# Performance work log

Measured on AMD Instinct MI355X. Metric: run time of the kernel, lower is better.

## Reference

```python
import jax, jax.numpy as jnp
import numpy as np

C = 1024
FACTOR = 4
C_INT = C * FACTOR


def setup_inputs() -> dict:
    key = jax.random.key(0)
    ks = jax.random.split(key, 6)
    act = jax.random.normal(ks[0], (4, 2048, C), dtype=jnp.float32)
    mask = jnp.ones((4, 2048), dtype=jnp.float32)
    # LayerNorm params
    ln_scale = jnp.ones((C,), dtype=jnp.float32)
    ln_bias = jnp.zeros((C,), dtype=jnp.float32)
    # Linear 1 (init='linear'): lecun-normal-ish
    w1 = jax.random.normal(ks[1], (C, C_INT), dtype=jnp.float32) / np.sqrt(C)
    b1 = jnp.zeros((C_INT,), dtype=jnp.float32)
    # Linear 2 (init='final' -> zeros in AF2; use small random so grads are nontrivial)
    w2 = jax.random.normal(ks[2], (C_INT, C), dtype=jnp.float32) * 0.02
    b2 = jnp.zeros((C,), dtype=jnp.float32)
    return {"act": act, "mask": mask, "ln_scale": ln_scale, "ln_bias": ln_bias,
            "w1": w1, "b1": b1, "w2": w2, "b2": b2}


def _layernorm(x, scale, bias, eps=1e-5):
    mu = jnp.mean(x, axis=-1, keepdims=True)
    var = jnp.mean(jnp.square(x - mu), axis=-1, keepdims=True)
    return (x - mu) * jax.lax.rsqrt(var + eps) * scale + bias


def reference(act, mask, ln_scale, ln_bias, w1, b1, w2, b2):
    # mask is accepted but unused, matching the original forward.
    x = _layernorm(act, ln_scale, ln_bias)
    h = jax.nn.relu(jnp.einsum('bsc,cf->bsf', x, w1) + b1)
    return jnp.einsum('bsf,fc->bsc', h, w2) + b2
```

## Files before the change

kernel.cpp:

```cpp
#include <hip/hip_runtime.h>
#include <hip/hip_bf16.h>
#include <cstdint>

typedef unsigned short u16;
typedef __bf16 bf16x8 __attribute__((ext_vector_type(8)));
typedef float floatx4 __attribute__((ext_vector_type(4)));

#define AS1 __attribute__((address_space(1)))
#define AS3 __attribute__((address_space(3)))

#define SCHED0  __builtin_amdgcn_sched_barrier(0)
#define BARRIER __builtin_amdgcn_s_barrier()

static __device__ __forceinline__ u16 f2bf(float f) {
    union { float f; unsigned int u; } v; v.f = f;
    unsigned int u = v.u;
    return (u16)((u + 0x7FFFu + ((u >> 16) & 1u)) >> 16);
}

__device__ __forceinline__ void transpose_body(
    const float* __restrict__ in, u16* __restrict__ out,
    int R, int Ccols, int bx, int by, int tid, float (*tile)[33])
{
    const int tx = tid & 31;
    const int ty = tid >> 5;
    const int c0 = bx * 32;
    const int r0 = by * 32;
#pragma unroll
    for (int i = 0; i < 32; i += 8)
        tile[ty + i][tx] = in[(size_t)(r0 + ty + i) * Ccols + (c0 + tx)];
    __syncthreads();
#pragma unroll
    for (int i = 0; i < 32; i += 8)
        out[(size_t)(c0 + ty + i) * R + (r0 + tx)] = f2bf(tile[tx][ty + i]);
}

__global__ __launch_bounds__(256)
void prep(const float* __restrict__ w1, const float* __restrict__ w2,
          const float* __restrict__ act, const float* __restrict__ ln_scale,
          const float* __restrict__ ln_bias,
          u16* __restrict__ W1t, u16* __restrict__ W2t, u16* __restrict__ X)
{
    __shared__ float smem[32][33];
    const int id  = blockIdx.x;
    const int tid = threadIdx.x;

    if (id < 4096) {
        transpose_body(w1, W1t, 1024, 4096, id & 127, id >> 7, tid, smem);
        return;
    }
    if (id < 8192) {
        const int t = id - 4096;
        transpose_body(w2, W2t, 4096, 1024, t & 31, t >> 5, tid, smem);
        return;
    }
    const int row = id - 8192;
    const float4 v = ((const float4*)(act + (size_t)row * 1024))[tid];
    float s  = v.x + v.y + v.z + v.w;
    float ss = v.x * v.x + v.y * v.y + v.z * v.z + v.w * v.w;
#pragma unroll
    for (int off = 32; off > 0; off >>= 1) {
        s  += __shfl_xor(s, off, 64);
        ss += __shfl_xor(ss, off, 64);
    }
    float* red = &smem[0][0];
    const int wave = tid >> 6, lane = tid & 63;
    if (lane == 0) { red[wave] = s; red[4 + wave] = ss; }
    __syncthreads();
    s  = red[0] + red[1] + red[2] + red[3];
    ss = red[4] + red[5] + red[6] + red[7];
    const float mu  = s * (1.0f / 1024.0f);
    const float var = ss * (1.0f / 1024.0f) - mu * mu;
    const float rs  = rsqrtf(var + 1e-5f);
    const float4 sc = ((const float4*)ln_scale)[tid];
    const float4 bi = ((const float4*)ln_bias)[tid];
    ushort4 o;
    o.x = f2bf((v.x - mu) * rs * sc.x + bi.x);
    o.y = f2bf((v.y - mu) * rs * sc.y + bi.y);
    o.z = f2bf((v.z - mu) * rs * sc.z + bi.z);
    o.w = f2bf((v.w - mu) * rs * sc.w + bi.w);
    ((ushort4*)(X + (size_t)row * 1024))[tid] = o;
}

__global__ __launch_bounds__(512, 2)
void gemm1(const u16* __restrict__ A, const u16* __restrict__ Bt,
           const float* __restrict__ bias, u16* __restrict__ H)
{
    constexpr int K = 1024, N = 4096;
    constexpr int ASZ = 256 * 64;
    __shared__ __align__(16) u16 Alds[2 * ASZ];
    __shared__ __align__(16) u16 Blds[2 * ASZ];

    const int tid  = threadIdx.x;
    const int wave = tid >> 6;
    const int lane = tid & 63;
    const int srow = lane >> 3;
    const int sst  = lane & 7;
    const int quad = lane >> 4;
    const int l16  = lane & 15;
    const int rkey = l16 & 7;
    const int wm   = wave >> 2;
    const int wn   = wave & 3;

    const int id = blockIdx.x;
    const int bm = id & 31;
    const int bn = id >> 5;

    const u16* Ag = A  + (size_t)bm * 256 * K;
    const u16* Bg = Bt + (size_t)bn * 256 * K;

    auto stA = [&](int buf, int c, int k0) {
        const int row = c * 64 + wave * 8 + srow;
        const int col = (sst ^ (row & 7)) * 8;
        __builtin_amdgcn_global_load_lds(
            (AS1 void*)(Ag + (size_t)row * K + k0 + col),
            (AS3 void*)(&Alds[buf * ASZ + c * 4096 + wave * 512]), 16, 0, 0);
    };
    auto stB = [&](int buf, int c, int k0) {
        const int row = c * 64 + wave * 8 + srow;
        const int col = (sst ^ (row & 7)) * 8;
        __builtin_amdgcn_global_load_lds(
            (AS1 void*)(Bg + (size_t)row * K + k0 + col),
            (AS3 void*)(&Blds[buf * ASZ + c * 4096 + wave * 512]), 16, 0, 0);
    };

    floatx4 acc[8][4];
#pragma unroll
    for (int i = 0; i < 8; ++i)
#pragma unroll
        for (int j = 0; j < 4; ++j)
            acc[i][j] = (floatx4){0.f, 0.f, 0.f, 0.f};

    constexpr int NT = K / 64;

    stA(0, 0, 0); stA(0, 2, 0);
    stB(0, 0, 0); stB(0, 1, 0); stB(0, 2, 0); stB(0, 3, 0);
    stA(0, 1, 0); stA(0, 3, 0);
    asm volatile("s_waitcnt vmcnt(2)" ::: "memory");
    SCHED0; BARRIER; SCHED0;

    bf16x8 bres[4][2];
    for (int t = 0; t < NT; ++t) {
        const int cb = t & 1, nb = cb ^ 1;
        const int ab = cb * ASZ, bb = cb * ASZ;
        const int k1 = (t + 1) * 64;
        const bool st = (t + 1 < NT);

#pragma unroll
        for (int p = 0; p < 4; ++p) {
            if (p == 0) {
#pragma unroll
                for (int ni = 0; ni < 4; ++ni) {
                    const int br = wn * 64 + ni * 16 + l16;
#pragma unroll
                    for (int kh = 0; kh < 2; ++kh)
                        bres[ni][kh] = *(const bf16x8*)
                            &Blds[bb + br * 64 + ((kh * 4 + quad) ^ rkey) * 8];
                }
            }
            bf16x8 afr[2][2];
#pragma unroll
            for (int j = 0; j < 2; ++j) {
                const int ar = wm * 128 + (2 * p + j) * 16 + l16;
#pragma unroll
                for (int kh = 0; kh < 2; ++kh)
                    afr[j][kh] = *(const bf16x8*)
                        &Alds[ab + ar * 64 + ((kh * 4 + quad) ^ rkey) * 8];
            }
            if (st) {
                if (p == 0)      { stA(nb, 0, k1); stA(nb, 2, k1); }
                else if (p == 1) { stB(nb, 0, k1); stB(nb, 1, k1); }
                else if (p == 2) { stB(nb, 2, k1); stB(nb, 3, k1); }
                else             { stA(nb, 1, k1); stA(nb, 3, k1); }
            }
            SCHED0; BARRIER;
            asm volatile("s_waitcnt lgkmcnt(0)" ::: "memory");
            SCHED0;
            __builtin_amdgcn_s_setprio(1);
#pragma unroll
            for (int kh = 0; kh < 2; ++kh)
#pragma unroll
                for (int j = 0; j < 2; ++j)
#pragma unroll
                    for (int ni = 0; ni < 4; ++ni)
                        acc[2 * p + j][ni] = __builtin_amdgcn_mfma_f32_16x16x32_bf16(
                            bres[ni][kh], afr[j][kh], acc[2 * p + j][ni], 0, 0, 0);
            __builtin_amdgcn_s_setprio(0);
            SCHED0;
            if (p == 1) {
                if (st) asm volatile("s_waitcnt vmcnt(4)" ::: "memory");
                else    asm volatile("s_waitcnt vmcnt(0)" ::: "memory");
            }
            if (p == 3 && st)
                asm volatile("s_waitcnt vmcnt(2)" ::: "memory");
            BARRIER; SCHED0;
        }
    }

    const int mbase = bm * 256 + wm * 128;
    const int nbase = bn * 256 + wn * 64;
#pragma unroll
    for (int mi = 0; mi < 8; ++mi) {
        const int m = mbase + mi * 16 + l16;
#pragma unroll
        for (int ni = 0; ni < 4; ++ni) {
            const int n0 = nbase + ni * 16 + quad * 4;
            const float4 bv = *(const float4*)&bias[n0];
            float v0 = fmaxf(acc[mi][ni][0] + bv.x, 0.f);
            float v1 = fmaxf(acc[mi][ni][1] + bv.y, 0.f);
            float v2 = fmaxf(acc[mi][ni][2] + bv.z, 0.f);
            float v3 = fmaxf(acc[mi][ni][3] + bv.w, 0.f);
            ushort4 o = { f2bf(v0), f2bf(v1), f2bf(v2), f2bf(v3) };
            *(ushort4*)&H[(size_t)m * N + n0] = o;
        }
    }
}

__global__ __launch_bounds__(512, 2)
void gemm2(const u16* __restrict__ A, const u16* __restrict__ Bt,
           const float* __restrict__ bias, float* __restrict__ Cout)
{
    constexpr int K = 4096, N = 1024;
    constexpr int ASZ = 2 * 256 * 32;
    constexpr int BSZ = 2 * 128 * 32;
    __shared__ __align__(16) u16 Alds[2 * ASZ];
    __shared__ __align__(16) u16 Blds[2 * BSZ];

    const int tid  = threadIdx.x;
    const int wave = tid >> 6;
    const int lane = tid & 63;
    const int quad = lane >> 4;
    const int l16  = lane & 15;
    const int key4 = (l16 >> 1) & 3;
    const int wm   = wave >> 1;
    const int wn   = wave & 1;

    const int id = blockIdx.x;
    const int bm = id & 31;
    const int bn = id >> 5;

    const u16* Ag = A  + (size_t)bm * 256 * K;
    const u16* Bg = Bt + (size_t)bn * 128 * K;

    auto stA = [&](int buf, int kh, int c, int k0) {
        const int row = c * 128 + wave * 16 + (lane >> 2);
        const int col = kh * 32 + ((lane & 3) ^ ((row >> 1) & 3)) * 8;
        __builtin_amdgcn_global_load_lds(
            (AS1 void*)(Ag + (size_t)row * K + k0 + col),
            (AS3 void*)(&Alds[buf * ASZ + kh * 8192 + c * 4096 + wave * 512]),
            16, 0, 0);
    };
    auto stB = [&](int buf, int kh, int k0) {
        const int row = wave * 16 + (lane >> 2);
        const int col = kh * 32 + ((lane & 3) ^ ((row >> 1) & 3)) * 8;
        __builtin_amdgcn_global_load_lds(
            (AS1 void*)(Bg + (size_t)row * K + k0 + col),
            (AS3 void*)(&Blds[buf * BSZ + kh * 4096 + wave * 512]), 16, 0, 0);
    };

    floatx4 acc[4][4];
#pragma unroll
    for (int i = 0; i < 4; ++i)
#pragma unroll
        for (int j = 0; j < 4; ++j)
            acc[i][j] = (floatx4){0.f, 0.f, 0.f, 0.f};

    constexpr int NT = K / 64;

    stA(0, 0, 0, 0); stA(0, 0, 1, 0); stB(0, 0, 0);
    stA(0, 1, 0, 0); stA(0, 1, 1, 0); stB(0, 1, 0);
    asm volatile("s_waitcnt vmcnt(3)" ::: "memory");
    SCHED0; BARRIER; SCHED0;

    for (int t = 0; t < NT; ++t) {
        const int cb = t & 1, nb = cb ^ 1;
        const int k1 = (t + 1) * 64;
        const bool st = (t + 1 < NT);

#pragma unroll
        for (int kh = 0; kh < 2; ++kh) {
            bf16x8 afr[4], bfr[4];
#pragma unroll
            for (int mi = 0; mi < 4; ++mi) {
                const int ar = wm * 64 + mi * 16 + l16;
                afr[mi] = *(const bf16x8*)
                    &Alds[cb * ASZ + kh * 8192 + ar * 32 + ((quad ^ key4) * 8)];
            }
#pragma unroll
            for (int ni = 0; ni < 4; ++ni) {
                const int br = wn * 64 + ni * 16 + l16;
                bfr[ni] = *(const bf16x8*)
                    &Blds[cb * BSZ + kh * 4096 + br * 32 + ((quad ^ key4) * 8)];
            }
            if (st) { stA(nb, kh, 0, k1); stA(nb, kh, 1, k1); stB(nb, kh, k1); }
            SCHED0; BARRIER;
            asm volatile("s_waitcnt lgkmcnt(0)" ::: "memory");
            SCHED0;
            __builtin_amdgcn_s_setprio(1);
#pragma unroll
            for (int mi = 0; mi < 4; ++mi)
#pragma unroll
                for (int ni = 0; ni < 4; ++ni)
                    acc[mi][ni] = __builtin_amdgcn_mfma_f32_16x16x32_bf16(
                        bfr[ni], afr[mi], acc[mi][ni], 0, 0, 0);
            __builtin_amdgcn_s_setprio(0);
            SCHED0;
            if (kh == 0) {
                if (st) asm volatile("s_waitcnt vmcnt(3)" ::: "memory");
                else    asm volatile("s_waitcnt vmcnt(0)" ::: "memory");
            } else if (st) {
                asm volatile("s_waitcnt vmcnt(3)" ::: "memory");
            }
            BARRIER; SCHED0;
        }
    }

    const int mbase = bm * 256 + wm * 64;
    const int nbase = bn * 128 + wn * 64;
#pragma unroll
    for (int mi = 0; mi < 4; ++mi) {
        const int m = mbase + mi * 16 + l16;
#pragma unroll
        for (int ni = 0; ni < 4; ++ni) {
            const int n0 = nbase + ni * 16 + quad * 4;
            const float4 bv = *(const float4*)&bias[n0];
            float4 o = { acc[mi][ni][0] + bv.x, acc[mi][ni][1] + bv.y,
                         acc[mi][ni][2] + bv.z, acc[mi][ni][3] + bv.w };
            *(float4*)&Cout[(size_t)m * N + n0] = o;
        }
    }
}

extern "C" void kernel_launch(void* const* d_in, const int* in_sizes, int n_in,
                              void* d_out, int out_size, void* d_ws, size_t ws_size,
                              hipStream_t stream)
{
    const float* act      = (const float*)d_in[0];
    const float* ln_scale = (const float*)d_in[2];
    const float* ln_bias  = (const float*)d_in[3];
    const float* w1       = (const float*)d_in[4];
    const float* b1       = (const float*)d_in[5];
    const float* w2       = (const float*)d_in[6];
    const float* b2       = (const float*)d_in[7];
    float* out = (float*)d_out;

    const int M = 8192, C = 1024, CI = 4096;

    u16* X   = (u16*)d_ws;
    u16* W1t = X   + (size_t)M * C;
    u16* W2t = W1t + (size_t)CI * C;
    u16* H   = W2t + (size_t)C * CI;

    prep<<<16384, 256, 0, stream>>>(w1, w2, act, ln_scale, ln_bias, W1t, W2t, X);
    gemm1<<<(M / 256) * (CI / 256), 512, 0, stream>>>(X, W1t, b1, H);
    gemm2<<<(M / 256) * (C / 128), 512, 0, stream>>>(H, W2t, b2, out);
}
```

Baseline: 268.2 us.

## Prefetch LDS fragments across barriers and triple-buffer gemm2 tiles

The weight transpose now handles 128x32 tiles per block with float4 loads and packed bf16x2 stores, which cuts the prep grid size. In gemm1, A/B fragment reads from LDS become raw ds_read_b128 with precomputed offsets, issued one phase ahead, with partial lgkmcnt waits instead of barrier-then-full-wait. gemm2 moves to a 3-stage LDS ring with register double-buffered fragments so loads for tile t+2 overlap MFMA on tile t. These are meant to hide LDS and global latency, in exchange for more LDS per block (which may lower occupancy) and fragile hand-tuned waitcnt accounting.

New measurement: 249.0 us. -7.2%, faster.

```diff
diff --git a/kernel.cpp b/kernel.cpp
--- a/kernel.cpp
+++ b/kernel.cpp
@@ -18,21 +18,36 @@
     return (u16)((u + 0x7FFFu + ((u >> 16) & 1u)) >> 16);
 }
 
+static __device__ __forceinline__ unsigned lds_off(const u16* p) {
+    return (unsigned)(unsigned long long)(const AS3 u16*)p;
+}
+static __device__ __forceinline__ bf16x8 ds_read8(unsigned off) {
+    bf16x8 r;
+    asm volatile("ds_read_b128 %0, %1" : "=v"(r) : "v"(off));
+    return r;
+}
+
 __device__ __forceinline__ void transpose_body(
     const float* __restrict__ in, u16* __restrict__ out,
     int R, int Ccols, int bx, int by, int tid, float (*tile)[33])
 {
-    const int tx = tid & 31;
-    const int ty = tid >> 5;
-    const int c0 = bx * 32;
-    const int r0 = by * 32;
-#pragma unroll
-    for (int i = 0; i < 32; i += 8)
-        tile[ty + i][tx] = in[(size_t)(r0 + ty + i) * Ccols + (c0 + tx)];
+    const int r0 = by * 128, c0 = bx * 32;
+#pragma unroll
+    for (int p = 0; p < 4; ++p) {
+        const int f = p * 256 + tid;
+        const int r = f >> 3, c4 = (f & 7) * 4;
+        const float4 v = *(const float4*)&in[(size_t)(r0 + r) * Ccols + c0 + c4];
+        tile[r][c4 + 0] = v.x; tile[r][c4 + 1] = v.y;
+        tile[r][c4 + 2] = v.z; tile[r][c4 + 3] = v.w;
+    }
     __syncthreads();
-#pragma unroll
-    for (int i = 0; i < 32; i += 8)
-        out[(size_t)(c0 + ty + i) * R + (r0 + tx)] = f2bf(tile[tx][ty + i]);
+    const int wv = tid >> 6, ln = tid & 63;
+#pragma unroll
+    for (int i = 0; i < 8; ++i) {
+        const int c = i * 4 + wv;
+        ushort2 o = { f2bf(tile[ln * 2][c]), f2bf(tile[ln * 2 + 1][c]) };
+        *(ushort2*)&out[(size_t)(c0 + c) * R + r0 + ln * 2] = o;
+    }
 }
 
 __global__ __launch_bounds__(256)
@@ -41,20 +56,20 @@
           const float* __restrict__ ln_bias,
           u16* __restrict__ W1t, u16* __restrict__ W2t, u16* __restrict__ X)
 {
-    __shared__ float smem[32][33];
+    __shared__ float tile[128][33];
     const int id  = blockIdx.x;
     const int tid = threadIdx.x;
 
-    if (id < 4096) {
-        transpose_body(w1, W1t, 1024, 4096, id & 127, id >> 7, tid, smem);
+    if (id < 1024) {
+        transpose_body(w1, W1t, 1024, 4096, id & 127, id >> 7, tid, tile);
         return;
     }
-    if (id < 8192) {
-        const int t = id - 4096;
-        transpose_body(w2, W2t, 4096, 1024, t & 31, t >> 5, tid, smem);
+    if (id < 2048) {
+        const int t = id - 1024;
+        transpose_body(w2, W2t, 4096, 1024, t & 31, t >> 5, tid, tile);
         return;
     }
-    const int row = id - 8192;
+    const int row = id - 2048;
     const float4 v = ((const float4*)(act + (size_t)row * 1024))[tid];
     float s  = v.x + v.y + v.z + v.w;
     float ss = v.x * v.x + v.y * v.y + v.z * v.z + v.w * v.w;
@@ -63,7 +78,7 @@
         s  += __shfl_xor(s, off, 64);
         ss += __shfl_xor(ss, off, 64);
     }
-    float* red = &smem[0][0];
+    float* red = &tile[0][0];
     const int wave = tid >> 6, lane = tid & 63;
     if (lane == 0) { red[wave] = s; red[4 + wave] = ss; }
     __syncthreads();
@@ -124,6 +139,22 @@
             (AS3 void*)(&Blds[buf * ASZ + c * 4096 + wave * 512]), 16, 0, 0);
     };
 
+    const unsigned Ab = lds_off(&Alds[0]);
+    const unsigned Bb = lds_off(&Blds[0]);
+    unsigned aoff[8][2], boff[4][2];
+#pragma unroll
+    for (int mi = 0; mi < 8; ++mi)
+#pragma unroll
+        for (int kh = 0; kh < 2; ++kh)
+            aoff[mi][kh] = ((wm * 128 + mi * 16 + l16) * 64 +
+                            ((kh * 4 + quad) ^ rkey) * 8) * 2;
+#pragma unroll
+    for (int ni = 0; ni < 4; ++ni)
+#pragma unroll
+        for (int kh = 0; kh < 2; ++kh)
+            boff[ni][kh] = ((wn * 64 + ni * 16 + l16) * 64 +
+                            ((kh * 4 + quad) ^ rkey) * 8) * 2;
+
     floatx4 acc[8][4];
 #pragma unroll
     for (int i = 0; i < 8; ++i)
@@ -140,9 +171,11 @@
     SCHED0; BARRIER; SCHED0;
 
     bf16x8 bres[4][2];
+    bf16x8 afr[2][2][2];
     for (int t = 0; t < NT; ++t) {
-        const int cb = t & 1, nb = cb ^ 1;
-        const int ab = cb * ASZ, bb = cb * ASZ;
+        const unsigned ab = Ab + (unsigned)((t & 1) * ASZ * 2);
+        const unsigned bb = Bb + (unsigned)((t & 1) * ASZ * 2);
+        const int nb = (t + 1) & 1;
         const int k1 = (t + 1) * 64;
         const bool st = (t + 1 < NT);
 
@@ -150,22 +183,24 @@
         for (int p = 0; p < 4; ++p) {
             if (p == 0) {
 #pragma unroll
-                for (int ni = 0; ni < 4; ++ni) {
-                    const int br = wn * 64 + ni * 16 + l16;
+                for (int ni = 0; ni < 4; ++ni)
 #pragma unroll
                     for (int kh = 0; kh < 2; ++kh)
-                        bres[ni][kh] = *(const bf16x8*)
-                            &Blds[bb + br * 64 + ((kh * 4 + quad) ^ rkey) * 8];
-                }
-            }
-            bf16x8 afr[2][2];
-#pragma unroll
-            for (int j = 0; j < 2; ++j) {
-                const int ar = wm * 128 + (2 * p + j) * 16 + l16;
-#pragma unroll
-                for (int kh = 0; kh < 2; ++kh)
-                    afr[j][kh] = *(const bf16x8*)
-                        &Alds[ab + ar * 64 + ((kh * 4 + quad) ^ rkey) * 8];
+                        bres[ni][kh] = ds_read8(bb + boff[ni][kh]);
+#pragma unroll
+                for (int sl = 0; sl < 2; ++sl)
+#pragma unroll
+                    for (int j = 0; j < 2; ++j)
+#pragma unroll
+                        for (int kh = 0; kh < 2; ++kh)
+                            afr[sl][j][kh] = ds_read8(ab + aoff[sl * 2 + j][kh]);
+            } else if (p < 3) {
+#pragma unroll
+                for (int j = 0; j < 2; ++j)
+#pragma unroll
+                    for (int kh = 0; kh < 2; ++kh)
+                        afr[(p + 1) & 1][j][kh] =
+                            ds_read8(ab + aoff[(p + 1) * 2 + j][kh]);
             }
             if (st) {
                 if (p == 0)      { stA(nb, 0, k1); stA(nb, 2, k1); }
@@ -173,8 +208,8 @@
                 else if (p == 2) { stB(nb, 2, k1); stB(nb, 3, k1); }
                 else             { stA(nb, 1, k1); stA(nb, 3, k1); }
             }
-            SCHED0; BARRIER;
-            asm volatile("s_waitcnt lgkmcnt(0)" ::: "memory");
+            if (p == 3) asm volatile("s_waitcnt lgkmcnt(0)" ::: "memory");
+            else        asm volatile("s_waitcnt lgkmcnt(4)" ::: "memory");
             SCHED0;
             __builtin_amdgcn_s_setprio(1);
 #pragma unroll
@@ -184,11 +219,11 @@
 #pragma unroll
                     for (int ni = 0; ni < 4; ++ni)
                         acc[2 * p + j][ni] = __builtin_amdgcn_mfma_f32_16x16x32_bf16(
-                            bres[ni][kh], afr[j][kh], acc[2 * p + j][ni], 0, 0, 0);
+                            bres[ni][kh], afr[p & 1][j][kh], acc[2 * p + j][ni], 0, 0, 0);
             __builtin_amdgcn_s_setprio(0);
             SCHED0;
-            if (p == 1) {
-                if (st) asm volatile("s_waitcnt vmcnt(4)" ::: "memory");
+            if (p == 0) {
+                if (st) asm volatile("s_waitcnt vmcnt(2)" ::: "memory");
                 else    asm volatile("s_waitcnt vmcnt(0)" ::: "memory");
             }
             if (p == 3 && st)
@@ -223,8 +258,8 @@
     constexpr int K = 4096, N = 1024;
     constexpr int ASZ = 2 * 256 * 32;
     constexpr int BSZ = 2 * 128 * 32;
-    __shared__ __align__(16) u16 Alds[2 * ASZ];
-    __shared__ __align__(16) u16 Blds[2 * BSZ];
+    __shared__ __align__(16) u16 Alds[3 * ASZ];
+    __shared__ __align__(16) u16 Blds[3 * BSZ];
 
     const int tid  = threadIdx.x;
     const int wave = tid >> 6;
@@ -258,6 +293,16 @@
             (AS3 void*)(&Blds[buf * BSZ + kh * 4096 + wave * 512]), 16, 0, 0);
     };
 
+    const unsigned Ab = lds_off(&Alds[0]);
+    const unsigned Bb = lds_off(&Blds[0]);
+    unsigned aoff[4], boff[4];
+#pragma unroll
+    for (int mi = 0; mi < 4; ++mi)
+        aoff[mi] = ((wm * 64 + mi * 16 + l16) * 32 + (quad ^ key4) * 8) * 2;
+#pragma unroll
+    for (int ni = 0; ni < 4; ++ni)
+        boff[ni] = ((wn * 64 + ni * 16 + l16) * 32 + (quad ^ key4) * 8) * 2;
+
     floatx4 acc[4][4];
 #pragma unroll
     for (int i = 0; i < 4; ++i)
@@ -267,52 +312,76 @@
 
     constexpr int NT = K / 64;
 
-    stA(0, 0, 0, 0); stA(0, 0, 1, 0); stB(0, 0, 0);
-    stA(0, 1, 0, 0); stA(0, 1, 1, 0); stB(0, 1, 0);
-    asm volatile("s_waitcnt vmcnt(3)" ::: "memory");
+    stA(0, 0, 0, 0);  stA(0, 0, 1, 0);  stB(0, 0, 0);
+    stA(0, 1, 0, 0);  stA(0, 1, 1, 0);  stB(0, 1, 0);
+    stA(1, 0, 0, 64); stA(1, 0, 1, 64); stB(1, 0, 64);
+    stA(1, 1, 0, 64); stA(1, 1, 1, 64); stB(1, 1, 64);
+    asm volatile("s_waitcnt vmcnt(6)" ::: "memory");
     SCHED0; BARRIER; SCHED0;
 
+    bf16x8 fa[2][4], fb[2][4];
+#pragma unroll
+    for (int i = 0; i < 4; ++i) {
+        fa[0][i] = ds_read8(Ab + aoff[i]);
+        fb[0][i] = ds_read8(Bb + boff[i]);
+    }
+
+    int bs0 = 0, bs1 = 1, bs2 = 2;
     for (int t = 0; t < NT; ++t) {
-        const int cb = t & 1, nb = cb ^ 1;
-        const int k1 = (t + 1) * 64;
-        const bool st = (t + 1 < NT);
-
-#pragma unroll
-        for (int kh = 0; kh < 2; ++kh) {
-            bf16x8 afr[4], bfr[4];
-#pragma unroll
-            for (int mi = 0; mi < 4; ++mi) {
-                const int ar = wm * 64 + mi * 16 + l16;
-                afr[mi] = *(const bf16x8*)
-                    &Alds[cb * ASZ + kh * 8192 + ar * 32 + ((quad ^ key4) * 8)];
+        const int k2 = (t + 2) * 64;
+        const bool st  = (t + 2 < NT);
+        const bool rd1 = (t + 1 < NT);
+        const unsigned a0 = Ab + (unsigned)(bs0 * ASZ * 2);
+        const unsigned b0 = Bb + (unsigned)(bs0 * BSZ * 2);
+        const unsigned a1 = Ab + (unsigned)(bs1 * ASZ * 2);
+        const unsigned b1 = Bb + (unsigned)(bs1 * BSZ * 2);
+
+#pragma unroll
+        for (int i = 0; i < 4; ++i) {
+            fa[1][i] = ds_read8(a0 + 16384u + aoff[i]);
+            fb[1][i] = ds_read8(b0 + 8192u  + boff[i]);
+        }
+        if (st) { stA(bs2, 0, 0, k2); stA(bs2, 0, 1, k2); stB(bs2, 0, k2); }
+        asm volatile("s_waitcnt lgkmcnt(8)" ::: "memory");
+        SCHED0;
+        __builtin_amdgcn_s_setprio(1);
+#pragma unroll
+        for (int mi = 0; mi < 4; ++mi)
+#pragma unroll
+            for (int ni = 0; ni < 4; ++ni)
+                acc[mi][ni] = __builtin_amdgcn_mfma_f32_16x16x32_bf16(
+                    fb[0][ni], fa[0][mi], acc[mi][ni], 0, 0, 0);
+        __builtin_amdgcn_s_setprio(0);
+        SCHED0;
+        if (st)       asm volatile("s_waitcnt vmcnt(6)" ::: "memory");
+        else if (rd1) asm volatile("s_waitcnt vmcnt(3)" ::: "memory");
+        BARRIER; SCHED0;
+
+        if (rd1) {
+#pragma unroll
+            for (int i = 0; i < 4; ++i) {
+                fa[0][i] = ds_read8(a1 + aoff[i]);
+                fb[0][i] = ds_read8(b1 + boff[i]);
             }
-#pragma unroll
-            for (int ni = 0; ni < 4; ++ni) {
-                const int br = wn * 64 + ni * 16 + l16;
-                bfr[ni] = *(const bf16x8*)
-                    &Blds[cb * BSZ + kh * 4096 + br * 32 + ((quad ^ key4) * 8)];
-            }
-            if (st) { stA(nb, kh, 0, k1); stA(nb, kh, 1, k1); stB(nb, kh, k1); }
-            SCHED0; BARRIER;
-            asm volatile("s_waitcnt lgkmcnt(0)" ::: "memory");
-            SCHED0;
-            __builtin_amdgcn_s_setprio(1);
-#pragma unroll
-            for (int mi = 0; mi < 4; ++mi)
-#pragma unroll
-                for (int ni = 0; ni < 4; ++ni)
-                    acc[mi][ni] = __builtin_amdgcn_mfma_f32_16x16x32_bf16(
-                        bfr[ni], afr[mi], acc[mi][ni], 0, 0, 0);
-            __builtin_amdgcn_s_setprio(0);
-            SCHED0;
-            if (kh == 0) {
-                if (st) asm volatile("s_waitcnt vmcnt(3)" ::: "memory");
-                else    asm volatile("s_waitcnt vmcnt(0)" ::: "memory");
-            } else if (st) {
-                asm volatile("s_waitcnt vmcnt(3)" ::: "memory");
-            }
-            BARRIER; SCHED0;
         }
+        if (st) { stA(bs2, 1, 0, k2); stA(bs2, 1, 1, k2); stB(bs2, 1, k2); }
+        if (rd1) asm volatile("s_waitcnt lgkmcnt(8)" ::: "memory");
+        else     asm volatile("s_waitcnt lgkmcnt(0)" ::: "memory");
+        SCHED0;
+        __builtin_amdgcn_s_setprio(1);
+#pragma unroll
+        for (int mi = 0; mi < 4; ++mi)
+#pragma unroll
+            for (int ni = 0; ni < 4; ++ni)
+                acc[mi][ni] = __builtin_amdgcn_mfma_f32_16x16x32_bf16(
+                    fb[1][ni], fa[1][mi], acc[mi][ni], 0, 0, 0);
+        __builtin_amdgcn_s_setprio(0);
+        SCHED0;
+        if (st)       asm volatile("s_waitcnt vmcnt(6)" ::: "memory");
+        else if (rd1) asm volatile("s_waitcnt vmcnt(0)" ::: "memory");
+        BARRIER; SCHED0;
+
+        const int tmp = bs0; bs0 = bs1; bs1 = bs2; bs2 = tmp;
     }
 
     const int mbase = bm * 256 + wm * 64;
@@ -351,7 +420,7 @@
     u16* W2t = W1t + (size_t)CI * C;
     u16* H   = W2t + (size_t)C * CI;
 
-    prep<<<16384, 256, 0, stream>>>(w1, w2, act, ln_scale, ln_bias, W1t, W2t, X);
+    prep<<<10240, 256, 0, stream>>>(w1, w2, act, ln_scale, ln_bias, W1t, W2t, X);
     gemm1<<<(M / 256) * (CI / 256), 512, 0, stream>>>(X, W1t, b1, H);
     gemm2<<<(M / 256) * (C / 128), 512, 0, stream>>>(H, W2t, b2, out);
 }
```
